# Kernel tuning notes

Measured on AMD Instinct MI355X. Metric: run time of the kernel, lower is better.

The kernel has to match this reference:

```python
import jax, jax.numpy as jnp
import numpy as np

N = 100000   # nodes
E = 1600000  # edges
F = 128      # input features
H = 128      # hidden
L = 4        # num_layers (1 conv1 + 3 convs)
S = 10000    # subgraphs
G = 256      # graphs
C = 10       # classes
BN_EPS = 1e-5


def setup_inputs() -> dict:
    key = jax.random.key(0)
    ks = jax.random.split(key, 12)
    x = jax.random.normal(ks[0], (N, F), jnp.float32)
    edge_index = jax.random.randint(ks[1], (2, E), 0, N, jnp.int32)
    node_to_subgraph = jnp.sort(jax.random.randint(ks[2], (N,), 0, S, jnp.int32))
    subgraph_to_graph = jnp.sort(jax.random.randint(ks[3], (S,), 0, G, jnp.int32))
    sc = 1.0 / np.sqrt(H)
    # stacked per-layer GIN MLP params (torch Linear layout [out, in]); F == H so conv1 stacks too
    W1 = jax.random.uniform(ks[4], (L, H, F), jnp.float32, -sc, sc)
    b1 = jax.random.uniform(ks[5], (L, H), jnp.float32, -sc, sc)
    g1 = jnp.ones((L, H), jnp.float32)
    be1 = jnp.zeros((L, H), jnp.float32)
    W2 = jax.random.uniform(ks[6], (L, H, H), jnp.float32, -sc, sc)
    b2 = jax.random.uniform(ks[7], (L, H), jnp.float32, -sc, sc)
    g2 = jnp.ones((L, H), jnp.float32)
    be2 = jnp.zeros((L, H), jnp.float32)
    eps = jnp.zeros((L,), jnp.float32)  # train_eps=True, init 0
    sc1 = 1.0 / np.sqrt(L * H)
    lin1_W = jax.random.uniform(ks[8], (H, L * H), jnp.float32, -sc1, sc1)
    lin1_b = jax.random.uniform(ks[9], (H,), jnp.float32, -sc1, sc1)
    lin2_W = jax.random.uniform(ks[10], (C, H), jnp.float32, -sc, sc)
    lin2_b = jax.random.uniform(ks[11], (C,), jnp.float32, -sc, sc)
    return dict(x=x, edge_index=edge_index, node_to_subgraph=node_to_subgraph,
                subgraph_to_graph=subgraph_to_graph, W1=W1, b1=b1, g1=g1, be1=be1,
                W2=W2, b2=b2, g2=g2, be2=be2, eps=eps,
                lin1_W=lin1_W, lin1_b=lin1_b, lin2_W=lin2_W, lin2_b=lin2_b)


def _bn(h, g, b):
    mu = h.mean(axis=0)
    var = jnp.mean((h - mu) ** 2, axis=0)  # biased var (training-mode BN)
    return (h - mu) * jax.lax.rsqrt(var + BN_EPS) * g + b


def _seg_mean(f, seg, num_segments):
    s = jax.ops.segment_sum(f, seg, num_segments=num_segments)
    cnt = jax.ops.segment_sum(jnp.ones((f.shape[0], 1), f.dtype), seg, num_segments=num_segments)
    return s / jnp.maximum(cnt, 1.0)


def reference(x, edge_index, node_to_subgraph, subgraph_to_graph,
              W1, b1, g1, be1, W2, b2, g2, be2, eps,
              lin1_W, lin1_b, lin2_W, lin2_b):
    src, dst = edge_index[0], edge_index[1]

    def layer(xc, p):
        w1, bb1, gg1, bt1, w2, bb2, gg2, bt2, e = p
        agg = jax.ops.segment_sum(xc[src], dst, num_segments=N)  # neighbor sum
        h = (1.0 + e) * xc + agg
        h = jax.nn.relu(_bn(h @ w1.T + bb1, gg1, bt1))
        h = jax.nn.relu(_bn(h @ w2.T + bb2, gg2, bt2))
        return h, h

    _, ys = jax.lax.scan(layer, x, (W1, b1, g1, be1, W2, b2, g2, be2, eps))  # [L, N, H]
    feat = jnp.transpose(ys, (1, 0, 2)).reshape(N, L * H)  # torch.cat(xs, dim=1)
    sub = _seg_mean(feat, node_to_subgraph, S)   # [S, L*H]
    gph = _seg_mean(sub, subgraph_to_graph, G)   # [G, L*H]
    h = jax.nn.relu(gph @ lin1_W.T + lin1_b)
    out = h @ lin2_W.T + lin2_b                  # dropout inactive in eval
    return jax.nn.log_softmax(out, axis=-1)
```

## Files before the change

kernel.cpp:

```cpp
#include <hip/hip_runtime.h>

typedef unsigned int u32;
typedef unsigned short u16;

#define NN 100000
#define EE 1600000
#define SS 10000
#define GG 256
#define NSCAN ((NN + 1023) / 1024)

#define O_W1   0
#define O_B1   65536
#define O_G1   66048
#define O_BE1  66560
#define O_W2   67072
#define O_B2   132608
#define O_G2   133120
#define O_BE2  133632
#define O_EPS  134144
#define O_L1W  134148
#define O_L1B  199684
#define O_L2W  199812
#define O_L2B  201092
#define NPAR   201102

typedef __bf16 bf16x8_t __attribute__((ext_vector_type(8)));
typedef float f32x4_t __attribute__((ext_vector_type(4)));
typedef u32 u32x4_t __attribute__((ext_vector_type(4)));

__device__ __forceinline__ float bf2f(u16 u) {
  union { u32 i; float f; } x; x.i = ((u32)u) << 16; return x.f;
}
__device__ __forceinline__ u16 f2bf(float f) {
  union { float f; u32 i; } x; x.f = f;
  u32 r = x.i + 0x7fffu + ((x.i >> 16) & 1u);
  return (u16)(r >> 16);
}
__device__ __forceinline__ int lbound(const int* __restrict__ a, int n, int key) {
  int lo = 0, hi = n;
  while (lo < hi) { int mid = (lo + hi) >> 1; if (a[mid] < key) lo = mid + 1; else hi = mid; }
  return lo;
}

__device__ __forceinline__ int local_sniff(const u16* x16, int t, int nthr, int* swc) {
  int w = 0;
  int per = 1024 / nthr;
  for (int k = 0; k < per; k++) {
    u16 v = x16[t + k * nthr];
    if (((v >> 7) & 0xff) >= 0xC0) w++;
  }
  atomicAdd(swc, w);
  __syncthreads();
  return (*swc > 16) ? 1 : 0;
}

__global__ __launch_bounds__(256) void k_setup(
    const void* __restrict__ x, const int* __restrict__ edst,
    const void* pW1, const void* pb1, const void* pg1, const void* pbe1,
    const void* pW2, const void* pb2, const void* pg2, const void* pbe2,
    const void* peps, const void* pl1w, const void* pl1b, const void* pl2w, const void* pl2b,
    float* __restrict__ P, u16* __restrict__ W1b, u16* __restrict__ W2b,
    u16* __restrict__ Z0, int* __restrict__ cnt) {
  __shared__ int swc;
  int t = threadIdx.x, b = blockIdx.x;
  if (t == 0) swc = 0;
  __syncthreads();
  int flag = local_sniff((const u16*)x, t, 256, &swc);

  int i = b * 256 + t;
  if (i < (NN * 128) / 8) {
    if (flag) {
      const float4* xf = (const float4*)x;
      float4 va = xf[i * 2], vb = xf[i * 2 + 1];
      u32x4_t o;
      o[0] = (u32)f2bf(va.x) | ((u32)f2bf(va.y) << 16);
      o[1] = (u32)f2bf(va.z) | ((u32)f2bf(va.w) << 16);
      o[2] = (u32)f2bf(vb.x) | ((u32)f2bf(vb.y) << 16);
      o[3] = (u32)f2bf(vb.z) | ((u32)f2bf(vb.w) << 16);
      *(u32x4_t*)(Z0 + i * 8) = o;
    } else {
      *(u32x4_t*)(Z0 + i * 8) = ((const u32x4_t*)x)[i];
    }
  }

  if (b < 512) {
    int j = b * 256 + t;
    if (j < 65536) W1b[j] = flag ? f2bf(((const float*)pW1)[j]) : ((const u16*)pW1)[j];
    else { int j2 = j - 65536; W2b[j2] = flag ? f2bf(((const float*)pW2)[j2]) : ((const u16*)pW2)[j2]; }
  } else if (b < 786) {
    int j = (b - 512) * 256 + t;
    if (j < 70030) {
      int i2 = (j < 1536) ? (O_B1 + j) : (O_B2 + (j - 1536));
      const void* src; int rel;
      if      (i2 < O_G1)  { src = pb1;  rel = i2 - O_B1; }
      else if (i2 < O_BE1) { src = pg1;  rel = i2 - O_G1; }
      else if (i2 < O_W2)  { src = pbe1; rel = i2 - O_BE1; }
      else if (i2 < O_G2)  { src = pb2;  rel = i2 - O_B2; }
      else if (i2 < O_BE2) { src = pg2;  rel = i2 - O_G2; }
      else if (i2 < O_EPS) { src = pbe2; rel = i2 - O_BE2; }
      else if (i2 < O_L1W) { src = peps; rel = i2 - O_EPS; }
      else if (i2 < O_L1B) { src = pl1w; rel = i2 - O_L1W; }
      else if (i2 < O_L2W) { src = pl1b; rel = i2 - O_L1B; }
      else if (i2 < O_L2B) { src = pl2w; rel = i2 - O_L2W; }
      else                 { src = pl2b; rel = i2 - O_L2B; }
      P[i2] = flag ? ((const float*)src)[rel] : bf2f(((const u16*)src)[rel]);
    }
  }

  int e = b * 256 + t;
  if (e < EE) atomicAdd(&cnt[edst[e]], 1);
}

__global__ __launch_bounds__(256) void k_scan1(const int* __restrict__ cnt, int* __restrict__ bsum) {
  __shared__ int sh[256];
  int base = blockIdx.x * 1024 + threadIdx.x * 4;
  int s = 0;
#pragma unroll
  for (int i = 0; i < 4; i++) { int idx = base + i; s += (idx < NN) ? cnt[idx] : 0; }
  sh[threadIdx.x] = s; __syncthreads();
  for (int o = 128; o > 0; o >>= 1) {
    if (threadIdx.x < o) sh[threadIdx.x] += sh[threadIdx.x + o];
    __syncthreads();
  }
  if (threadIdx.x == 0) bsum[blockIdx.x] = sh[0];
}

__global__ __launch_bounds__(256) void k_scan3x(const int* __restrict__ cnt, const int* __restrict__ bsum,
                                                int* __restrict__ off) {
  __shared__ int sh[256];
  __shared__ int bpre;
  if (threadIdx.x < 64) {
    int l = threadIdx.x;
    int v = 0;
    if (l < blockIdx.x && l < NSCAN) v += bsum[l];
    if (l + 64 < blockIdx.x && l + 64 < NSCAN) v += bsum[l + 64];
    for (int o = 1; o < 64; o <<= 1) v += __shfl_xor(v, o, 64);
    if (l == 0) bpre = v;
  }
  int base = blockIdx.x * 1024 + threadIdx.x * 4;
  int v4[4]; int s = 0;
#pragma unroll
  for (int i = 0; i < 4; i++) { int idx = base + i; v4[i] = (idx < NN) ? cnt[idx] : 0; s += v4[i]; }
  sh[threadIdx.x] = s; __syncthreads();
  for (int o = 1; o < 256; o <<= 1) {
    int add = (threadIdx.x >= o) ? sh[threadIdx.x - o] : 0;
    __syncthreads();
    sh[threadIdx.x] += add;
    __syncthreads();
  }
  int run = sh[threadIdx.x] - s + bpre;
#pragma unroll
  for (int i = 0; i < 4; i++) {
    int idx = base + i;
    if (idx < NN) { off[idx] = run; run += v4[i]; if (idx == NN - 1) off[NN] = run; }
  }
}

__global__ __launch_bounds__(256) void k_fill(const int* __restrict__ src, const int* __restrict__ dst,
                                              const int* __restrict__ off, int* __restrict__ cur,
                                              int* __restrict__ csr) {
  int i = blockIdx.x * 256 + threadIdx.x;
  if (i >= EE) return;
  int d = dst[i];
  int p = off[d] + atomicAdd(&cur[d], 1);
  csr[p] = src[i];
}

__global__ __launch_bounds__(256) void k_agg_gemm(
    const u16* __restrict__ Z, const int* __restrict__ off, const int* __restrict__ csr,
    const u16* __restrict__ Wb, const float* __restrict__ bias, const float* __restrict__ P,
    int layer, u16* __restrict__ H, float* __restrict__ st) {
  __shared__ __align__(16) u16 lds[4][16][136];
  __shared__ __align__(16) int shidx[4][512];
  int wave = threadIdx.x >> 6, lane = threadIdx.x & 63;
  int r0 = blockIdx.x * 64 + wave * 16;
  float ev = 1.0f + P[O_EPS + layer];
  const u32* zr = (const u32*)Z;

  int offv = 0;
  if (lane <= 16) {
    int rr = r0 + lane; if (rr > NN) rr = NN; if (rr < 0) rr = 0;
    offv = off[rr];
  }
  int ebase = __shfl(offv, 0, 64);
  int eend  = __shfl(offv, 16, 64);
  int tn = eend - ebase;
  int nst = tn < 512 ? tn : 512;
  for (int i = lane; i < nst; i += 64) shidx[wave][i] = csr[ebase + i];

  for (int rr = 0; rr < 16; rr++) {
    int row = r0 + rr;
    float a0 = 0.f, a1 = 0.f;
    if (row < NN) {
      int s = __shfl(offv, rr, 64), e = __shfl(offv, rr + 1, 64);
      int n = e - s, b = s - ebase;
      u32 d = zr[row * 64 + lane];
      a0 = ev * bf2f((u16)(d & 0xffffu));
      a1 = ev * bf2f((u16)(d >> 16));
      const int* ip = (b + n <= 512) ? &shidx[wave][b] : &csr[s];
      int i = 0;
      for (; i + 7 < n; i += 8) {
        u32 dd[8];
#pragma unroll
        for (int j = 0; j < 8; j++) dd[j] = zr[ip[i + j] * 64 + lane];
#pragma unroll
        for (int j = 0; j < 8; j++) {
          a0 += bf2f((u16)(dd[j] & 0xffffu));
          a1 += bf2f((u16)(dd[j] >> 16));
        }
      }
      for (; i + 1 < n; i += 2) {
        u32 d0 = zr[ip[i] * 64 + lane];
        u32 d1 = zr[ip[i + 1] * 64 + lane];
        a0 += bf2f((u16)(d0 & 0xffffu)) + bf2f((u16)(d1 & 0xffffu));
        a1 += bf2f((u16)(d0 >> 16)) + bf2f((u16)(d1 >> 16));
      }
      if (i < n) {
        u32 d0 = zr[ip[i] * 64 + lane];
        a0 += bf2f((u16)(d0 & 0xffffu));
        a1 += bf2f((u16)(d0 >> 16));
      }
    }
    ((u32*)&lds[wave][rr][0])[lane] = (u32)f2bf(a0) | ((u32)f2bf(a1) << 16);
  }

  int nidx = lane & 15, q = lane >> 4;
  f32x4_t acc[8];
  f32x4_t z4 = {0.f, 0.f, 0.f, 0.f};
#pragma unroll
  for (int ot = 0; ot < 8; ot++) acc[ot] = z4;
#pragma unroll
  for (int ks = 0; ks < 4; ks++) {
    bf16x8_t af = __builtin_bit_cast(bf16x8_t, *(const u32x4_t*)&lds[wave][nidx][ks * 32 + q * 8]);
#pragma unroll
    for (int ot = 0; ot < 8; ot++) {
      bf16x8_t bfr = __builtin_bit_cast(bf16x8_t, *(const u32x4_t*)(Wb + (ot * 16 + nidx) * 128 + ks * 32 + q * 8));
      acc[ot] = __builtin_amdgcn_mfma_f32_16x16x32_bf16(af, bfr, acc[ot], 0, 0, 0);
    }
  }
  float* sstw = (float*)&shidx[wave][0];
#pragma unroll
  for (int ot = 0; ot < 8; ot++) {
    int col = ot * 16 + nidx;
    float bv = bias[col];
    float s = 0.f, sq = 0.f;
#pragma unroll
    for (int j = 0; j < 4; j++) {
      int row = r0 + q * 4 + j;
      if (row < NN) {
        float v = acc[ot][j] + bv;
        u16 h = f2bf(v);
        float vr = bf2f(h);
        H[row * 128 + col] = h;
        s += vr; sq += vr * vr;
      }
    }
    s  += __shfl_xor(s, 16, 64);  s  += __shfl_xor(s, 32, 64);
    sq += __shfl_xor(sq, 16, 64); sq += __shfl_xor(sq, 32, 64);
    if (q == 0) { sstw[col] = s; sstw[128 + col] = sq; }
  }
  __syncthreads();
  int t = threadIdx.x;
  float tot = ((float*)&shidx[0][0])[t] + ((float*)&shidx[1][0])[t] +
              ((float*)&shidx[2][0])[t] + ((float*)&shidx[3][0])[t];
  atomicAdd(&st[t], tot);
}

__global__ __launch_bounds__(256) void k_bn_gemm(
    const u16* __restrict__ Hin, const u16* __restrict__ Wb, const float* __restrict__ bias,
    const float* __restrict__ st_in, const float* __restrict__ gw, const float* __restrict__ bw,
    u16* __restrict__ Hout, float* __restrict__ st_out) {
  __shared__ float sc[256];
  __shared__ float sst[4][256];
  int t = threadIdx.x;
  if (t < 128) {
    float mu = st_in[t] * (1.0f / NN);
    float var = st_in[128 + t] * (1.0f / NN) - mu * mu;
    var = fmaxf(var, 0.f);
    float r = rsqrtf(var + 1e-5f);
    float scl = gw[t] * r;
    sc[t] = scl;
    sc[128 + t] = bw[t] - mu * scl;
  }
  __syncthreads();
  int wave = t >> 6, lane = t & 63;
  int r0 = blockIdx.x * 64 + wave * 16;
  int nidx = lane & 15, q = lane >> 4;
  int arow = r0 + nidx;
  u32x4_t zero4 = {0, 0, 0, 0};
  u32x4_t raw[4];
#pragma unroll
  for (int ks = 0; ks < 4; ks++)
    raw[ks] = (arow < NN) ? *(const u32x4_t*)(Hin + arow * 128 + ks * 32 + q * 8) : zero4;
  f32x4_t acc[8];
  f32x4_t z4 = {0.f, 0.f, 0.f, 0.f};
#pragma unroll
  for (int ot = 0; ot < 8; ot++) acc[ot] = z4;
#pragma unroll
  for (int ks = 0; ks < 4; ks++) {
    int k0 = ks * 32 + q * 8;
    u32x4_t ap;
#pragma unroll
    for (int w = 0; w < 4; w++) {
      int k = k0 + 2 * w;
      float v0 = fmaxf(bf2f((u16)(raw[ks][w] & 0xffffu)) * sc[k] + sc[128 + k], 0.f);
      float v1 = fmaxf(bf2f((u16)(raw[ks][w] >> 16)) * sc[k + 1] + sc[128 + k + 1], 0.f);
      ap[w] = (u32)f2bf(v0) | ((u32)f2bf(v1) << 16);
    }
    bf16x8_t af = __builtin_bit_cast(bf16x8_t, ap);
#pragma unroll
    for (int ot = 0; ot < 8; ot++) {
      bf16x8_t bfr = __builtin_bit_cast(bf16x8_t, *(const u32x4_t*)(Wb + (ot * 16 + nidx) * 128 + k0));
      acc[ot] = __builtin_amdgcn_mfma_f32_16x16x32_bf16(af, bfr, acc[ot], 0, 0, 0);
    }
  }
#pragma unroll
  for (int ot = 0; ot < 8; ot++) {
    int col = ot * 16 + nidx;
    float bv = bias[col];
    float s = 0.f, sq = 0.f;
#pragma unroll
    for (int j = 0; j < 4; j++) {
      int row = r0 + q * 4 + j;
      if (row < NN) {
        float v = acc[ot][j] + bv;
        u16 h = f2bf(v);
        float vr = bf2f(h);
        Hout[row * 128 + col] = h;
        s += vr; sq += vr * vr;
      }
    }
    s  += __shfl_xor(s, 16, 64);  s  += __shfl_xor(s, 32, 64);
    sq += __shfl_xor(sq, 16, 64); sq += __shfl_xor(sq, 32, 64);
    if (q == 0) { sst[wave][col] = s; sst[wave][128 + col] = sq; }
  }
  __syncthreads();
  float tot = sst[0][t] + sst[1][t] + sst[2][t] + sst[3][t];
  atomicAdd(&st_out[t], tot);
}

__global__ __launch_bounds__(256) void k_bn_sub(
    const u16* __restrict__ Hin, const float* __restrict__ st_in, const float* __restrict__ gw,
    const float* __restrict__ bw, const int* __restrict__ n2s,
    u16* __restrict__ Znext, float* __restrict__ sub, int layer) {
  __shared__ float sc[256];
  int t = threadIdx.x;
  if (t < 128) {
    float mu = st_in[t] * (1.0f / NN);
    float var = st_in[128 + t] * (1.0f / NN) - mu * mu;
    var = fmaxf(var, 0.f);
    float r = rsqrtf(var + 1e-5f);
    float scl = gw[t] * r;
    sc[t] = scl;
    sc[128 + t] = bw[t] - mu * scl;
  }
  __syncthreads();
  int s = (blockIdx.x * 256 + t) >> 6;
  int lane = t & 63;
  if (s >= SS) return;
  int r0 = lbound(n2s, NN, s), r1 = lbound(n2s, NN, s + 1);
  float scl0 = sc[2 * lane], scl1 = sc[2 * lane + 1];
  float sh0 = sc[128 + 2 * lane], sh1 = sc[128 + 2 * lane + 1];
  const u32* hr = (const u32*)Hin;
  u32* zr = (u32*)Znext;
  float a0 = 0.f, a1 = 0.f;
  for (int r = r0; r < r1; r++) {
    u32 d = hr[r * 64 + lane];
    float v0 = fmaxf(bf2f((u16)(d & 0xffffu)) * scl0 + sh0, 0.f);
    float v1 = fmaxf(bf2f((u16)(d >> 16)) * scl1 + sh1, 0.f);
    zr[r * 64 + lane] = (u32)f2bf(v0) | ((u32)f2bf(v1) << 16);
    a0 += v0; a1 += v1;
  }
  int c = r1 - r0;
  float inv = 1.0f / (float)(c > 0 ? c : 1);
  float2 v; v.x = a0 * inv; v.y = a1 * inv;
  *(float2*)(sub + (size_t)s * 512 + layer * 128 + lane * 2) = v;
}

__global__ __launch_bounds__(128) void k_poolhead(const float* __restrict__ sub, const int* __restrict__ s2g,
                                                  const float* __restrict__ P, const void* __restrict__ x,
                                                  void* __restrict__ out) {
  __shared__ float gsh[512];
  __shared__ float hsh[128];
  __shared__ float lsh[12];
  __shared__ int swc;
  int g = blockIdx.x, t = threadIdx.x;
  if (t == 0) swc = 0;
  __syncthreads();
  int flag = local_sniff((const u16*)x, t, 128, &swc);

  int r0 = lbound(s2g, SS, g), r1 = lbound(s2g, SS, g + 1);
  float4 a = {0.f, 0.f, 0.f, 0.f};
  for (int s = r0; s < r1; s++) {
    float4 v = ((const float4*)(sub + (size_t)s * 512))[t];
    a.x += v.x; a.y += v.y; a.z += v.z; a.w += v.w;
  }
  int c = r1 - r0;
  float inv = 1.0f / (float)(c > 0 ? c : 1);
  float4 sc4; sc4.x = a.x * inv; sc4.y = a.y * inv; sc4.z = a.z * inv; sc4.w = a.w * inv;
  *(float4*)(gsh + t * 4) = sc4;
  __syncthreads();

  float acc = P[O_L1B + t];
  const float4* wr = (const float4*)(P + O_L1W + t * 512);
  for (int kb = 0; kb < 128; kb++) {
    float4 w = wr[kb];
    int k = kb * 4;
    acc += gsh[k] * w.x + gsh[k + 1] * w.y + gsh[k + 2] * w.z + gsh[k + 3] * w.w;
  }
  hsh[t] = fmaxf(acc, 0.f);
  __syncthreads();
  if (t < 10) {
    float aa = P[O_L2B + t];
    const float* w2r = P + O_L2W + t * 128;
    for (int k = 0; k < 128; k++) aa += hsh[k] * w2r[k];
    lsh[t] = aa;
  }
  __syncthreads();
  if (t == 0) {
    float m = -1e30f;
    for (int cc = 0; cc < 10; cc++) m = fmaxf(m, lsh[cc]);
    float se = 0.f;
    for (int cc = 0; cc < 10; cc++) se += expf(lsh[cc] - m);
    lsh[10] = m + logf(se);
  }
  __syncthreads();
  if (t < 10) {
    float v = lsh[t] - lsh[10];
    if (flag) ((float*)out)[g * 10 + t] = v;
    else      ((u16*)out)[g * 10 + t] = f2bf(v);
  }
}

extern "C" void kernel_launch(void* const* d_in, const int* in_sizes, int n_in,
                              void* d_out, int out_size, void* d_ws, size_t ws_size,
                              hipStream_t stream) {
  const void* x   = d_in[0];
  const int* ei   = (const int*)d_in[1];
  const int* n2s  = (const int*)d_in[2];
  const int* s2g  = (const int*)d_in[3];

  char* ws = (char*)d_ws;
  size_t o = 0;
  auto alloc = [&](size_t b) -> void* {
    void* p = ws + o;
    o += (b + 255) & ~(size_t)255;
    return p;
  };
  int* off    = (int*)alloc((NN + 1) * 4);
  int* cnt    = (int*)alloc(NN * 4);
  int* cur    = (int*)alloc(NN * 4);
  float* stats = (float*)alloc(8 * 256 * 4);
  int* bsum   = (int*)alloc(NSCAN * 4);
  int* csr    = (int*)alloc((size_t)EE * 4);
  u16* zb0    = (u16*)alloc((size_t)NN * 128 * 2);
  u16* zb1    = (u16*)alloc((size_t)NN * 128 * 2);
  u16* H1     = (u16*)alloc((size_t)NN * 128 * 2);
  u16* H2     = (u16*)alloc((size_t)NN * 128 * 2);
  float* sub  = (float*)alloc((size_t)SS * 512 * 4);
  float* P    = (float*)alloc((size_t)NPAR * 4);
  u16* W1b    = (u16*)alloc(65536 * 2);
  u16* W2b    = (u16*)alloc(65536 * 2);

  const int* esrc = ei;
  const int* edst = ei + EE;

  size_t zspan = (char*)(stats + 8 * 256) - (char*)cnt;
  hipMemsetAsync(cnt, 0, zspan, stream);

  k_setup<<<dim3(6250), dim3(256), 0, stream>>>(
      x, edst,
      d_in[4], d_in[5], d_in[6], d_in[7], d_in[8], d_in[9], d_in[10], d_in[11],
      d_in[12], d_in[13], d_in[14], d_in[15], d_in[16],
      P, W1b, W2b, zb0, cnt);

  k_scan1<<<dim3(NSCAN), dim3(256), 0, stream>>>(cnt, bsum);
  k_scan3x<<<dim3(NSCAN), dim3(256), 0, stream>>>(cnt, bsum, off);
  k_fill<<<dim3((EE + 255) / 256), dim3(256), 0, stream>>>(esrc, edst, off, cur, csr);

  for (int l = 0; l < 4; l++) {
    const u16* Zin = (l == 0) ? zb0 : ((l & 1) ? zb1 : zb0);
    u16* Zout = (l & 1) ? zb0 : zb1;
    float* st1 = stats + (2 * l) * 256;
    float* st2 = stats + (2 * l + 1) * 256;
    k_agg_gemm<<<dim3((NN + 63) / 64), dim3(256), 0, stream>>>(
        Zin, off, csr, W1b + l * 16384, P + O_B1 + l * 128, P, l, H1, st1);
    k_bn_gemm<<<dim3((NN + 63) / 64), dim3(256), 0, stream>>>(
        H1, W2b + l * 16384, P + O_B2 + l * 128, st1, P + O_G1 + l * 128, P + O_BE1 + l * 128, H2, st2);
    k_bn_sub<<<dim3((SS + 3) / 4), dim3(256), 0, stream>>>(
        H2, st2, P + O_G2 + l * 128, P + O_BE2 + l * 128, n2s, Zout, sub, l);
  }
  k_poolhead<<<dim3(GG), dim3(128), 0, stream>>>(sub, s2g, P, x, (void*)d_out);
}
```

Before: 1.186 ms.

## Pipeline neighbor gathers via async global-to-LDS loads across a wave's edge list

Rewrites the neighbor aggregation in the fused agg+GEMM kernel to flatten all edges of a wave's 16 rows into one stream. It issues direct global-to-LDS loads into a triple-buffered staging area, keeping 16 row loads in flight and flushing per-row sums into LDS at row boundaries. The aim is to hide gather latency that the old per-row loop exposed, especially for short rows. The cost is extra LDS (24 KB per block), which may reduce occupancy. The self term is now rounded to bf16 before the neighbours are added, which slightly changes rounding.

```diff
diff --git a/kernel.cpp b/kernel.cpp
--- a/kernel.cpp
+++ b/kernel.cpp
@@ -52,6 +52,12 @@
   atomicAdd(swc, w);
   __syncthreads();
   return (*swc > 16) ? 1 : 0;
+}
+
+__device__ __forceinline__ void issue_row(const u32* __restrict__ zr, u32 idx, int lane, u32* slot) {
+  __builtin_amdgcn_global_load_lds(
+      (const __attribute__((address_space(1))) u32*)(zr + (size_t)idx * 64 + lane),
+      (__attribute__((address_space(3))) u32*)slot, 4, 0, 0);
 }
 
 __global__ __launch_bounds__(256) void k_setup(
@@ -171,6 +177,7 @@
     const u16* __restrict__ Wb, const float* __restrict__ bias, const float* __restrict__ P,
     int layer, u16* __restrict__ H, float* __restrict__ st) {
   __shared__ __align__(16) u16 lds[4][16][136];
+  __shared__ __align__(16) u32 stag[4][24][64];
   __shared__ __align__(16) int shidx[4][512];
   int wave = threadIdx.x >> 6, lane = threadIdx.x & 63;
   int r0 = blockIdx.x * 64 + wave * 16;
@@ -179,50 +186,111 @@
 
   int offv = 0;
   if (lane <= 16) {
-    int rr = r0 + lane; if (rr > NN) rr = NN; if (rr < 0) rr = 0;
-    offv = off[rr];
+    int rr2 = r0 + lane; if (rr2 > NN) rr2 = NN; if (rr2 < 0) rr2 = 0;
+    offv = off[rr2];
   }
   int ebase = __shfl(offv, 0, 64);
   int eend  = __shfl(offv, 16, 64);
   int tn = eend - ebase;
-  int nst = tn < 512 ? tn : 512;
-  for (int i = lane; i < nst; i += 64) shidx[wave][i] = csr[ebase + i];
-
-  for (int rr = 0; rr < 16; rr++) {
-    int row = r0 + rr;
-    float a0 = 0.f, a1 = 0.f;
-    if (row < NN) {
-      int s = __shfl(offv, rr, 64), e = __shfl(offv, rr + 1, 64);
-      int n = e - s, b = s - ebase;
-      u32 d = zr[row * 64 + lane];
-      a0 = ev * bf2f((u16)(d & 0xffffu));
-      a1 = ev * bf2f((u16)(d >> 16));
-      const int* ip = (b + n <= 512) ? &shidx[wave][b] : &csr[s];
-      int i = 0;
-      for (; i + 7 < n; i += 8) {
-        u32 dd[8];
-#pragma unroll
-        for (int j = 0; j < 8; j++) dd[j] = zr[ip[i + j] * 64 + lane];
-#pragma unroll
-        for (int j = 0; j < 8; j++) {
-          a0 += bf2f((u16)(dd[j] & 0xffffu));
-          a1 += bf2f((u16)(dd[j] >> 16));
+
+  for (int rr2 = 0; rr2 < 16; rr2++) {
+    int row = r0 + rr2;
+    u32 d = (row < NN) ? zr[row * 64 + lane] : 0u;
+    float s0 = ev * bf2f((u16)(d & 0xffffu));
+    float s1 = ev * bf2f((u16)(d >> 16));
+    ((u32*)&lds[wave][rr2][0])[lane] = (u32)f2bf(s0) | ((u32)f2bf(s1) << 16);
+  }
+
+#define FLUSH(RR) {                                                        \
+    u32 dcur = ((u32*)&lds[wave][RR][0])[lane];                            \
+    float s0 = bf2f((u16)(dcur & 0xffffu)) + a0;                           \
+    float s1 = bf2f((u16)(dcur >> 16)) + a1;                               \
+    ((u32*)&lds[wave][RR][0])[lane] = (u32)f2bf(s0) | ((u32)f2bf(s1) << 16); \
+    a0 = 0.f; a1 = 0.f; }
+
+  if (tn <= 512) {
+    for (int i = lane; i < tn; i += 64) shidx[wave][i] = csr[ebase + i];
+
+    int G = (tn + 7) >> 3;
+    for (int g = 0; g < 3; g++) {
+#pragma unroll
+      for (int k = 0; k < 8; k++) {
+        int j2 = g * 8 + k;
+        u32 idxk = (j2 < tn) ? (u32)shidx[wave][j2] : 0u;
+        issue_row(zr, idxk, lane, &stag[wave][g * 8 + k][0]);
+      }
+    }
+    int rr = 0; float a0 = 0.f, a1 = 0.f;
+    int rowend = __shfl(offv, 1, 64) - ebase;
+    int rg = 0;
+    for (int g = 0; g < G; g++) {
+      asm volatile("s_waitcnt vmcnt(16)" ::: "memory");
+      u32 dv[8];
+#pragma unroll
+      for (int k = 0; k < 8; k++) dv[k] = stag[wave][rg * 8 + k][lane];
+      asm volatile("" ::: "memory");
+      {
+        int jb = (g + 3) * 8;
+#pragma unroll
+        for (int k = 0; k < 8; k++) {
+          int j2 = jb + k;
+          u32 idxk = (j2 < tn) ? (u32)shidx[wave][j2] : 0u;
+          issue_row(zr, idxk, lane, &stag[wave][rg * 8 + k][0]);
         }
       }
-      for (; i + 1 < n; i += 2) {
-        u32 d0 = zr[ip[i] * 64 + lane];
-        u32 d1 = zr[ip[i + 1] * 64 + lane];
-        a0 += bf2f((u16)(d0 & 0xffffu)) + bf2f((u16)(d1 & 0xffffu));
-        a1 += bf2f((u16)(d0 >> 16)) + bf2f((u16)(d1 >> 16));
+      int jb0 = g * 8;
+      int kmax = tn - jb0; if (kmax > 8) kmax = 8;
+      for (int k = 0; k < kmax; k++) {
+        int j = jb0 + k;
+        while (j == rowend && rr < 15) {
+          FLUSH(rr);
+          rr++;
+          rowend = __shfl(offv, rr + 1, 64) - ebase;
+        }
+        a0 += bf2f((u16)(dv[k] & 0xffffu));
+        a1 += bf2f((u16)(dv[k] >> 16));
       }
-      if (i < n) {
-        u32 d0 = zr[ip[i] * 64 + lane];
-        a0 += bf2f((u16)(d0 & 0xffffu));
-        a1 += bf2f((u16)(d0 >> 16));
+      rg = (rg == 2) ? 0 : rg + 1;
+    }
+    FLUSH(rr);
+  } else {
+    for (int rr2 = 0; rr2 < 16; rr2++) {
+      int row = r0 + rr2;
+      float a0 = 0.f, a1 = 0.f;
+      if (row < NN) {
+        int s = __shfl(offv, rr2, 64), e = __shfl(offv, rr2 + 1, 64);
+        int n = e - s;
+        u32 d = zr[row * 64 + lane];
+        a0 = ev * bf2f((u16)(d & 0xffffu));
+        a1 = ev * bf2f((u16)(d >> 16));
+        const int* ip = &csr[s];
+        int i = 0;
+        for (; i + 7 < n; i += 8) {
+          u32 dd[8];
+#pragma unroll
+          for (int j = 0; j < 8; j++) dd[j] = zr[ip[i + j] * 64 + lane];
+#pragma unroll
+          for (int j = 0; j < 8; j++) {
+            a0 += bf2f((u16)(dd[j] & 0xffffu));
+            a1 += bf2f((u16)(dd[j] >> 16));
+          }
+        }
+        for (; i + 1 < n; i += 2) {
+          u32 d0 = zr[ip[i] * 64 + lane];
+          u32 d1 = zr[ip[i + 1] * 64 + lane];
+          a0 += bf2f((u16)(d0 & 0xffffu)) + bf2f((u16)(d1 & 0xffffu));
+          a1 += bf2f((u16)(d0 >> 16)) + bf2f((u16)(d1 >> 16));
+        }
+        if (i < n) {
+          u32 d0 = zr[ip[i] * 64 + lane];
+          a0 += bf2f((u16)(d0 & 0xffffu));
+          a1 += bf2f((u16)(d0 >> 16));
+        }
       }
-    }
-    ((u32*)&lds[wave][rr][0])[lane] = (u32)f2bf(a0) | ((u32)f2bf(a1) << 16);
-  }
+      ((u32*)&lds[wave][rr2][0])[lane] = (u32)f2bf(a0) | ((u32)f2bf(a1) << 16);
+    }
+  }
+#undef FLUSH
 
   int nidx = lane & 15, q = lane >> 4;
   f32x4_t acc[8];
```

After: 1.518 ms. 1.28x slower.
